# Performance work log

Measured on AMD Instinct MI355X. Metric: run time of the kernel, lower is better.

## Reference

```python
import jax, jax.numpy as jnp
import numpy as np

BN_EPS = 1e-3  # Keras BatchNormalization default epsilon


def setup_inputs() -> dict:
    key = jax.random.key(0)
    ks = jax.random.split(key, 5)
    B, H, W, C = 8, 64, 64, 256
    c = C // 4  # downsize_factor = 4
    OC = 256
    return {
        "x": jax.random.normal(ks[0], (B, H, W, C), dtype=jnp.float32),
        "Wk": jax.random.normal(ks[1], (C, c), dtype=jnp.float32) * 0.05,
        "Wq": jax.random.normal(ks[2], (C, c), dtype=jnp.float32) * 0.05,
        "Wv": jax.random.normal(ks[3], (C, c), dtype=jnp.float32) * 0.05,
        "Wo": jax.random.normal(ks[4], (c, OC), dtype=jnp.float32) * 0.05,
        "gamma": jnp.ones((OC,), dtype=jnp.float32),
        "beta": jnp.zeros((OC,), dtype=jnp.float32),
        "moving_mean": jnp.zeros((OC,), dtype=jnp.float32),
        "moving_var": jnp.ones((OC,), dtype=jnp.float32),
    }


def reference(x, Wk, Wq, Wv, Wo, gamma, beta, moving_mean, moving_var):
    B, H, W, C = x.shape
    c = Wk.shape[1]
    # 1x1 convs (no bias) == per-position matmuls; flatten spatial to N = H*W
    xf = x.reshape(B, H * W, C)
    k = xf @ Wk  # [B, N, c]
    q = xf @ Wq  # [B, N, c]
    v = xf @ Wv  # [B, N, c]
    # Keras Dot(axes=2)([key, query]): scores[b,i,j] = sum_c k[b,i,c]*q[b,j,c]  (unscaled)
    scores = jnp.einsum('bic,bjc->bij', k, q)  # [B, N, N]
    attn = jax.nn.softmax(scores, axis=-1)
    # Dot(axes=(2,1))([attn, value])
    out = jnp.einsum('bij,bjc->bic', attn, v)  # [B, N, c]
    out = out.reshape(B, H, W, c)
    # output 1x1 conv
    out = jnp.einsum('bhwc,co->bhwo', out, Wo)
    # BatchNorm (inference, moving statistics)
    out = gamma * (out - moving_mean) * jax.lax.rsqrt(moving_var + BN_EPS) + beta
    return out
```

## Files before the change

### kernel.cpp

```cpp
#include <hip/hip_runtime.h>
#include <hip/hip_bf16.h>

typedef __bf16 bf16_8 __attribute__((ext_vector_type(8)));
typedef _Float16 f16x8 __attribute__((ext_vector_type(8)));
typedef float f32x4 __attribute__((ext_vector_type(4)));
typedef float f32x16 __attribute__((ext_vector_type(16)));

#define MFMA_BF(A, B, C)    __builtin_amdgcn_mfma_f32_16x16x32_bf16(A, B, C, 0, 0, 0)
#define MFMA_F16(A, B, C)   __builtin_amdgcn_mfma_f32_16x16x32_f16(A, B, C, 0, 0, 0)
#define MFMA32_F16(A, B, C) __builtin_amdgcn_mfma_f32_32x32x16_f16(A, B, C, 0, 0, 0)
#define MFMA32_BF(A, B, C)  __builtin_amdgcn_mfma_f32_32x32x16_bf16(A, B, C, 0, 0, 0)

#define BATCH 8
#define NPOS 4096
#define CIN 256
#define CMID 64
#define OC 256
#define NROWS (BATCH * NPOS)
#define NSPLIT 4
#define LOG2E 1.44269504088896f

__device__ inline void swaplane32(unsigned& a, unsigned& b) {
    asm volatile("v_permlane32_swap_b32 %0, %1" : "+v"(a), "+v"(b));
}

#if __has_builtin(__builtin_amdgcn_exp2f)
__device__ inline float fexp2(float x) { return __builtin_amdgcn_exp2f(x); }
#else
__device__ inline float fexp2(float x) {
    float r;
    asm("v_exp_f32 %0, %1\n\ts_nop 1" : "=v"(r) : "v"(x));
    return r;
}
#endif

__global__ __launch_bounds__(256) void proj_kernel(
    const float* __restrict__ x,
    const float* __restrict__ Wk, const float* __restrict__ Wq,
    const float* __restrict__ Wv,
    _Float16* __restrict__ k_ws, _Float16* __restrict__ q_ws,
    __bf16* __restrict__ vT_ws)
{
    const int m = blockIdx.y;
    const int r0 = blockIdx.x * 64;
    const float* W = (m == 0) ? Wk : (m == 1) ? Wq : Wv;
    const float wscale = (m == 0) ? LOG2E : 1.0f;

    __shared__ _Float16 wt[64][266];

    for (int idx = threadIdx.x; idx < 64 * 256; idx += 256) {
        int col = idx & 63, k = idx >> 6;
        wt[col][k] = (_Float16)(W[k * 64 + col] * wscale);
    }

    const int lane = threadIdx.x & 63;
    const int wv = threadIdx.x >> 6;
    const int kbase = ((lane >> 4) & 3) * 8;
    const int arow = r0 + wv * 16 + (lane & 15);
    const float* xrow = x + (size_t)arow * CIN;

    f16x8 a[8];
    #pragma unroll
    for (int kk = 0; kk < 8; ++kk) {
        const float4* xp = (const float4*)(xrow + kk * 32 + kbase);
        float4 x0 = xp[0], x1 = xp[1];
        float xs[8] = {x0.x, x0.y, x0.z, x0.w, x1.x, x1.y, x1.z, x1.w};
        #pragma unroll
        for (int e = 0; e < 8; ++e) a[kk][e] = (_Float16)xs[e];
    }
    __syncthreads();

    f32x4 acc[4] = {f32x4{0,0,0,0}, f32x4{0,0,0,0}, f32x4{0,0,0,0}, f32x4{0,0,0,0}};
    #pragma unroll
    for (int kk = 0; kk < 8; ++kk) {
        #pragma unroll
        for (int nt = 0; nt < 4; ++nt) {
            f16x8 b = *(const f16x8*)&wt[(lane & 15) + 16 * nt][kk * 32 + kbase];
            acc[nt] = MFMA_F16(a[kk], b, acc[nt]);
        }
    }

    const int rloc = wv * 16 + ((lane >> 4) & 3) * 4;
    if (m < 2) {
        __syncthreads();
        _Float16* rp = &wt[0][0];
        #pragma unroll
        for (int nt = 0; nt < 4; ++nt)
            #pragma unroll
            for (int r = 0; r < 4; ++r)
                rp[(rloc + r) * 72 + (lane & 15) + 16 * nt] = (_Float16)acc[nt][r];
        __syncthreads();
        _Float16* dst = (m == 0) ? k_ws : q_ws;
        const int row = threadIdx.x >> 3, c0 = (threadIdx.x & 7) * 8;
        #pragma unroll
        for (int h = 0; h < 2; ++h) {
            uint4 v = *(const uint4*)&rp[(row + 32 * h) * 72 + c0];
            *(uint4*)(dst + (size_t)(r0 + row + 32 * h) * CMID + c0) = v;
        }
    } else {
        const int rrow = r0 + rloc;
        const int b = rrow >> 12;
        const int n = rrow & (NPOS - 1);
        #pragma unroll
        for (int nt = 0; nt < 4; ++nt) {
            int cv = (lane & 15) + 16 * nt;
            union { __bf16 h[4]; uint2 u; } pk;
            #pragma unroll
            for (int r = 0; r < 4; ++r) pk.h[r] = (__bf16)acc[nt][r];
            *(uint2*)(vT_ws + ((size_t)b * CMID + cv) * NPOS + n) = pk.u;
        }
    }
}

__global__ __launch_bounds__(512, 4) void flash_kernel(
    const _Float16* __restrict__ k_ws,
    const _Float16* __restrict__ q_ws,
    const __bf16* __restrict__ vT_ws,
    __bf16* __restrict__ po,
    float* __restrict__ pden)
{
    const int b = blockIdx.y;
    const int i0 = blockIdx.x * 256;
    const int sblk = blockIdx.z;
    const int jbase = sblk * (NPOS / NSPLIT);
    const int lane = threadIdx.x & 63;
    const int wv = threadIdx.x >> 6;
    const int l31 = lane & 31;
    const int g = lane >> 5;

    __shared__ _Float16 qt[2][64][72];
    __shared__ __bf16 vt[2][64][72];

    f16x8 kf[4];
    {
        const _Float16* kp =
            k_ws + ((size_t)(b * NPOS + i0 + wv * 32 + l31)) * CMID + g * 8;
        #pragma unroll
        for (int c = 0; c < 4; ++c) kf[c] = *(const f16x8*)(kp + c * 16);
    }

    f32x16 o0 = {0,0,0,0,0,0,0,0,0,0,0,0,0,0,0,0};
    f32x16 o1 = {0,0,0,0,0,0,0,0,0,0,0,0,0,0,0,0};
    float den = 0.f;

    const int r = threadIdx.x >> 3, c0 = (threadIdx.x & 7) * 8;
    uint4 nq, nv;

    {
        nq = *(const uint4*)(q_ws + ((size_t)(b * NPOS + jbase + r)) * CMID + c0);
        nv = *(const uint4*)(vT_ws + ((size_t)b * CMID + r) * NPOS + jbase + c0);
        *(uint4*)&qt[0][r][c0] = nq;
        *(uint4*)&vt[0][r][c0] = nv;
    }
    __syncthreads();

    const int NT = (NPOS / NSPLIT) / 64;
    for (int t = 0; t < NT; ++t) {
        const int cur = t & 1;
        if (t + 1 < NT) {
            int j1 = jbase + (t + 1) * 64;
            nq = *(const uint4*)(q_ws + ((size_t)(b * NPOS + j1 + r)) * CMID + c0);
            nv = *(const uint4*)(vT_ws + ((size_t)b * CMID + r) * NPOS + j1 + c0);
        }

        #pragma unroll
        for (int jj = 0; jj < 2; ++jj) {
            f16x8 aq[4];
            #pragma unroll
            for (int c = 0; c < 4; ++c)
                aq[c] = *(const f16x8*)&qt[cur][jj * 32 + l31][c * 16 + g * 8];
            bf16_8 bv00 = *(const bf16_8*)&vt[cur][l31][jj * 32 + g * 8];
            bf16_8 bv01 = *(const bf16_8*)&vt[cur][l31][jj * 32 + 16 + g * 8];
            bf16_8 bv10 = *(const bf16_8*)&vt[cur][32 + l31][jj * 32 + g * 8];
            bf16_8 bv11 = *(const bf16_8*)&vt[cur][32 + l31][jj * 32 + 16 + g * 8];

            f32x16 s = {0,0,0,0,0,0,0,0,0,0,0,0,0,0,0,0};
            s = MFMA32_F16(aq[0], kf[0], s);
            s = MFMA32_F16(aq[1], kf[1], s);
            s = MFMA32_F16(aq[2], kf[2], s);
            s = MFMA32_F16(aq[3], kf[3], s);

            unsigned pk[8];
            #pragma unroll
            for (int m = 0; m < 8; ++m) {
                float p0 = fexp2(s[2 * m]);
                float p1 = fexp2(s[2 * m + 1]);
                den += p0 + p1;
                union { __bf16 h[2]; unsigned u; } w;
                w.h[0] = (__bf16)p0; w.h[1] = (__bf16)p1;
                pk[m] = w.u;
            }
            swaplane32(pk[0], pk[2]); swaplane32(pk[1], pk[3]);
            swaplane32(pk[4], pk[6]); swaplane32(pk[5], pk[7]);
            union { unsigned u[4]; bf16_8 v; } pa0, pa1;
            pa0.u[0] = pk[0]; pa0.u[1] = pk[1]; pa0.u[2] = pk[2]; pa0.u[3] = pk[3];
            pa1.u[0] = pk[4]; pa1.u[1] = pk[5]; pa1.u[2] = pk[6]; pa1.u[3] = pk[7];

            o0 = MFMA32_BF(pa0.v, bv00, o0);
            o0 = MFMA32_BF(pa1.v, bv01, o0);
            o1 = MFMA32_BF(pa0.v, bv10, o1);
            o1 = MFMA32_BF(pa1.v, bv11, o1);
        }

        if (t + 1 < NT) {
            const int nb = cur ^ 1;
            *(uint4*)&qt[nb][r][c0] = nq;
            *(uint4*)&vt[nb][r][c0] = nv;
        }
        __syncthreads();
    }

    den += __shfl_xor(den, 32);

    const size_t rowb = (size_t)b * NPOS + i0 + wv * 32;
    if (lane < 32)
        pden[(size_t)sblk * NROWS + rowb + lane] = den;

    #pragma unroll
    for (int reg = 0; reg < 16; ++reg) {
        int il = (reg & 3) + 8 * (reg >> 2) + 4 * g;
        size_t base = ((size_t)sblk * NROWS + rowb + il) * CMID + l31;
        po[base]      = (__bf16)o0[reg];
        po[base + 32] = (__bf16)o1[reg];
    }
}

__global__ __launch_bounds__(256) void out_kernel(
    const __bf16* __restrict__ po,
    const float* __restrict__ pden,
    const float* __restrict__ Wo,
    const float* __restrict__ gamma, const float* __restrict__ beta,
    const float* __restrict__ mmean, const float* __restrict__ mvar,
    float* __restrict__ out)
{
    const int r0 = blockIdx.x * 16;
    const int t = threadIdx.x;
    const int lane = t & 63;
    const int wv = t >> 6;
    const int n0 = wv * 64;

    __shared__ __bf16 at[16][72];
    __shared__ float dinv[16];
    __shared__ float ot[16][260];

    bf16_8 wb[4][2];
    #pragma unroll
    for (int nt = 0; nt < 4; ++nt) {
        int col = n0 + nt * 16 + (lane & 15);
        #pragma unroll
        for (int ch = 0; ch < 2; ++ch)
            #pragma unroll
            for (int e = 0; e < 8; ++e)
                wb[nt][ch][e] = (__bf16)Wo[(ch * 32 + (lane >> 4) * 8 + e) * OC + col];
    }

    if (t < 16) {
        float d = 0.f;
        #pragma unroll
        for (int s = 0; s < NSPLIT; ++s) d += pden[(size_t)s * NROWS + r0 + t];
        dinv[t] = 1.0f / d;
    }
    __syncthreads();

    for (int idx = t; idx < 16 * 64; idx += 256) {
        int rr = idx >> 6, c = idx & 63;
        float sum = 0.f;
        #pragma unroll
        for (int s = 0; s < NSPLIT; ++s)
            sum += (float)po[((size_t)s * NROWS + r0 + rr) * CMID + c];
        at[rr][c] = (__bf16)(sum * dinv[rr]);
    }
    __syncthreads();

    bf16_8 a0 = *(const bf16_8*)&at[lane & 15][(lane >> 4) * 8];
    bf16_8 a1 = *(const bf16_8*)&at[lane & 15][32 + (lane >> 4) * 8];

    #pragma unroll
    for (int nt = 0; nt < 4; ++nt) {
        int col = n0 + nt * 16 + (lane & 15);
        f32x4 acc = {0.f, 0.f, 0.f, 0.f};
        acc = MFMA_BF(a0, wb[nt][0], acc);
        acc = MFMA_BF(a1, wb[nt][1], acc);
        float sc = gamma[col] * rsqrtf(mvar[col] + 1e-3f);
        float sh = beta[col] - mmean[col] * sc;
        int rl = (lane >> 4) * 4;
        #pragma unroll
        for (int rr = 0; rr < 4; ++rr)
            ot[rl + rr][col] = acc[rr] * sc + sh;
    }
    __syncthreads();

    {
        const int sr = t >> 6;
        const int sc4 = (t & 63) * 4;
        #pragma unroll
        for (int p = 0; p < 4; ++p) {
            int row = p * 4 + sr;
            float4 v = *(const float4*)&ot[row][sc4];
            *(float4*)&out[(size_t)(r0 + row) * OC + sc4] = v;
        }
    }
}

extern "C" void kernel_launch(void* const* d_in, const int* in_sizes, int n_in,
                              void* d_out, int out_size, void* d_ws, size_t ws_size,
                              hipStream_t stream) {
    const float* x     = (const float*)d_in[0];
    const float* Wk    = (const float*)d_in[1];
    const float* Wq    = (const float*)d_in[2];
    const float* Wv    = (const float*)d_in[3];
    const float* Wo    = (const float*)d_in[4];
    const float* gamma = (const float*)d_in[5];
    const float* beta  = (const float*)d_in[6];
    const float* mmean = (const float*)d_in[7];
    const float* mvar  = (const float*)d_in[8];
    float* out = (float*)d_out;

    char* ob = (char*)d_out;
    const size_t MB4 = (size_t)NROWS * CMID * 2;
    _Float16* k_ws = (_Float16*)ob;
    _Float16* q_ws = (_Float16*)(ob + MB4);
    __bf16*   vT   = (__bf16*)(ob + 2 * MB4);

    __bf16* po   = (__bf16*)d_ws;
    float*  pden = (float*)((char*)d_ws + (size_t)NSPLIT * MB4);

    proj_kernel<<<dim3(512, 3), 256, 0, stream>>>(x, Wk, Wq, Wv, k_ws, q_ws, vT);
    flash_kernel<<<dim3(16, 8, NSPLIT), 512, 0, stream>>>(k_ws, q_ws, vT, po, pden);
    out_kernel<<<2048, 256, 0, stream>>>(po, pden, Wo, gamma, beta, mmean, mvar, out);
}
```

Before: 89.98 us.

## Process 64 rows per out_kernel block and write output directly from MFMA

The output-projection kernel now handles 64 rows per block instead of 16, so the bf16 Wo fragments and the BatchNorm scale and shift, now hoisted into registers, are reused across four row groups. Partial sums are read as 4-wide vector loads. The shared-memory staging of results is removed and each lane stores its MFMA outputs straight to global memory. This cuts redundant weight loads and one barrier, but the direct stores are scattered 4-byte writes rather than coalesced float4 rows, and the grid shrinks to 512 blocks.

```diff
diff --git a/kernel.cpp b/kernel.cpp
--- a/kernel.cpp
+++ b/kernel.cpp
@@ -233,15 +233,14 @@
     const float* __restrict__ mmean, const float* __restrict__ mvar,
     float* __restrict__ out)
 {
-    const int r0 = blockIdx.x * 16;
+    const int r0 = blockIdx.x * 64;
     const int t = threadIdx.x;
     const int lane = t & 63;
     const int wv = t >> 6;
     const int n0 = wv * 64;
 
-    __shared__ __bf16 at[16][72];
-    __shared__ float dinv[16];
-    __shared__ float ot[16][260];
+    __shared__ __bf16 at[64][72];
+    __shared__ float dinv[64];
 
     bf16_8 wb[4][2];
     #pragma unroll
@@ -254,7 +253,15 @@
                 wb[nt][ch][e] = (__bf16)Wo[(ch * 32 + (lane >> 4) * 8 + e) * OC + col];
     }
 
-    if (t < 16) {
+    float scs[4], shs[4];
+    #pragma unroll
+    for (int nt = 0; nt < 4; ++nt) {
+        int col = n0 + nt * 16 + (lane & 15);
+        scs[nt] = gamma[col] * rsqrtf(mvar[col] + 1e-3f);
+        shs[nt] = beta[col] - mmean[col] * scs[nt];
+    }
+
+    if (t < 64) {
         float d = 0.f;
         #pragma unroll
         for (int s = 0; s < NSPLIT; ++s) d += pden[(size_t)s * NROWS + r0 + t];
@@ -262,42 +269,40 @@
     }
     __syncthreads();
 
-    for (int idx = t; idx < 16 * 64; idx += 256) {
-        int rr = idx >> 6, c = idx & 63;
-        float sum = 0.f;
-        #pragma unroll
-        for (int s = 0; s < NSPLIT; ++s)
-            sum += (float)po[((size_t)s * NROWS + r0 + rr) * CMID + c];
-        at[rr][c] = (__bf16)(sum * dinv[rr]);
+    #pragma unroll
+    for (int q = 0; q < 4; ++q) {
+        int quad = t + q * 256;
+        int rr = quad >> 4, c4 = (quad & 15) * 4;
+        float s0 = 0.f, s1 = 0.f, s2 = 0.f, s3 = 0.f;
+        #pragma unroll
+        for (int s = 0; s < NSPLIT; ++s) {
+            union { uint2 u; __bf16 h[4]; } qq;
+            qq.u = *(const uint2*)&po[((size_t)s * NROWS + r0 + rr) * CMID + c4];
+            s0 += (float)qq.h[0]; s1 += (float)qq.h[1];
+            s2 += (float)qq.h[2]; s3 += (float)qq.h[3];
+        }
+        float di = dinv[rr];
+        union { __bf16 h[4]; uint2 u; } o;
+        o.h[0] = (__bf16)(s0 * di); o.h[1] = (__bf16)(s1 * di);
+        o.h[2] = (__bf16)(s2 * di); o.h[3] = (__bf16)(s3 * di);
+        *(uint2*)&at[rr][c4] = o.u;
     }
     __syncthreads();
 
-    bf16_8 a0 = *(const bf16_8*)&at[lane & 15][(lane >> 4) * 8];
-    bf16_8 a1 = *(const bf16_8*)&at[lane & 15][32 + (lane >> 4) * 8];
-
-    #pragma unroll
-    for (int nt = 0; nt < 4; ++nt) {
-        int col = n0 + nt * 16 + (lane & 15);
-        f32x4 acc = {0.f, 0.f, 0.f, 0.f};
-        acc = MFMA_BF(a0, wb[nt][0], acc);
-        acc = MFMA_BF(a1, wb[nt][1], acc);
-        float sc = gamma[col] * rsqrtf(mvar[col] + 1e-3f);
-        float sh = beta[col] - mmean[col] * sc;
-        int rl = (lane >> 4) * 4;
-        #pragma unroll
-        for (int rr = 0; rr < 4; ++rr)
-            ot[rl + rr][col] = acc[rr] * sc + sh;
-    }
-    __syncthreads();
-
-    {
-        const int sr = t >> 6;
-        const int sc4 = (t & 63) * 4;
-        #pragma unroll
-        for (int p = 0; p < 4; ++p) {
-            int row = p * 4 + sr;
-            float4 v = *(const float4*)&ot[row][sc4];
-            *(float4*)&out[(size_t)(r0 + row) * OC + sc4] = v;
+    #pragma unroll
+    for (int rg = 0; rg < 4; ++rg) {
+        bf16_8 a0 = *(const bf16_8*)&at[rg * 16 + (lane & 15)][(lane >> 4) * 8];
+        bf16_8 a1 = *(const bf16_8*)&at[rg * 16 + (lane & 15)][32 + (lane >> 4) * 8];
+        #pragma unroll
+        for (int nt = 0; nt < 4; ++nt) {
+            int col = n0 + nt * 16 + (lane & 15);
+            f32x4 acc = {0.f, 0.f, 0.f, 0.f};
+            acc = MFMA_BF(a0, wb[nt][0], acc);
+            acc = MFMA_BF(a1, wb[nt][1], acc);
+            int rl = rg * 16 + (lane >> 4) * 4;
+            #pragma unroll
+            for (int rr = 0; rr < 4; ++rr)
+                out[(size_t)(r0 + rl + rr) * OC + col] = acc[rr] * scs[nt] + shs[nt];
         }
     }
 }
@@ -327,5 +332,5 @@
 
     proj_kernel<<<dim3(512, 3), 256, 0, stream>>>(x, Wk, Wq, Wv, k_ws, q_ws, vT);
     flash_kernel<<<dim3(16, 8, NSPLIT), 512, 0, stream>>>(k_ws, q_ws, vT, po, pden);
-    out_kernel<<<2048, 256, 0, stream>>>(po, pden, Wo, gamma, beta, mmean, mvar, out);
-}
+    out_kernel<<<512, 256, 0, stream>>>(po, pden, Wo, gamma, beta, mmean, mvar, out);
+}
```

New measurement: 85.17 us. 1.06x faster.
